# Optimization experiments

Hardware: AMD Instinct MI355X
Metric: run time of the kernel (lower is better)

## Reference

```python
import jax, jax.numpy as jnp
import numpy as np

STATE_DIM = 32
CONTROL_DIM = 8
EMBED_DIM = 96
LATENT_DIM = STATE_DIM + EMBED_DIM  # 128
HIDDEN = 512
B, M = 2048, 64


def setup_inputs() -> dict:
    key = jax.random.key(0)
    ks = jax.random.split(key, 16)
    s = lambda k, shp, fan: jax.random.normal(k, shp, jnp.float32) * (1.0 / np.sqrt(fan))
    return {
        "x_k": jax.random.normal(ks[0], (B, STATE_DIM), jnp.float32),
        "u_seq": jax.random.normal(ks[1], (B, M, CONTROL_DIM), jnp.float32),
        "x_next_seq": jax.random.normal(ks[2], (B, M, STATE_DIM), jnp.float32),
        # encoder MLP (depth=3): in->h, h->h, h->h, h->embed
        "W1": s(ks[3], (STATE_DIM, HIDDEN), STATE_DIM), "b1": jnp.zeros((HIDDEN,), jnp.float32),
        "W2": s(ks[4], (HIDDEN, HIDDEN), HIDDEN), "b2": jnp.zeros((HIDDEN,), jnp.float32),
        "W3": s(ks[5], (HIDDEN, HIDDEN), HIDDEN), "b3": jnp.zeros((HIDDEN,), jnp.float32),
        "Wo": s(ks[6], (HIDDEN, EMBED_DIM), HIDDEN), "bo": jnp.zeros((EMBED_DIM,), jnp.float32),
        # Koopman operators (Linear, no bias); stored as [in, out]
        "A": s(ks[7], (LATENT_DIM, LATENT_DIM), LATENT_DIM),
        "Bmat": s(ks[8], (CONTROL_DIM, LATENT_DIM), CONTROL_DIM),
    }


def _encode(x, W1, b1, W2, b2, W3, b3, Wo, bo):
    h = jax.nn.relu(x @ W1 + b1)
    h = jax.nn.relu(h @ W2 + b2)
    h = jax.nn.relu(h @ W3 + b3)
    return h @ Wo + bo


def _lift(x, W1, b1, W2, b2, W3, b3, Wo, bo):
    return jnp.concatenate([x, _encode(x, W1, b1, W2, b2, W3, b3, Wo, bo)], axis=-1)


def reference(x_k, u_seq, x_next_seq, W1, b1, W2, b2, W3, b3, Wo, bo, A, Bmat):
    m = u_seq.shape[1]
    z_k = _lift(x_k, W1, b1, W2, b2, W3, b3, Wo, bo)  # [B, L]
    # lift targets (encoder applied to flattened [B*M, S])
    z_target_seq = _lift(x_next_seq.reshape(-1, STATE_DIM), W1, b1, W2, b2, W3, b3, Wo, bo)
    z_target_seq = z_target_seq.reshape(-1, m, LATENT_DIM)
    # precompute control contributions, then sequential LTI recurrence via scan
    bu = jnp.einsum('bmc,cl->mbl', u_seq, Bmat)  # [M, B, L]

    def step(z, bu_i):
        z_next = z @ A + bu_i
        return z_next, z_next

    _, z_pred = jax.lax.scan(step, z_k, bu)  # [M, B, L]
    z_pred_seq = jnp.transpose(z_pred, (1, 0, 2))  # [B, M, L]
    x_pred_seq = z_pred_seq[..., :STATE_DIM]
    return (z_pred_seq, x_pred_seq, z_target_seq)
```

## Files before the change

kernel.cpp:

```cpp
#include <hip/hip_runtime.h>


typedef unsigned short u16;
typedef __attribute__((ext_vector_type(8))) short bf16x8;
typedef __attribute__((ext_vector_type(4))) short bf16x4;
typedef __attribute__((ext_vector_type(4))) float f32x4;

#define OFF_W1 0
#define OFF_W2 16384
#define OFF_W3 278528
#define OFF_WO 540672
#define OFF_ZK_BYTES 1179648
#define OFF_AH 1114112
#define OFF_AL 1130496

#define XPRED_OFF 16777216
#define ZTGT_OFF  20971520

__device__ __forceinline__ float bf2f(u16 u) {
  unsigned int i = ((unsigned int)u) << 16;
  return __builtin_bit_cast(float, i);
}
__device__ __forceinline__ u16 f2bf(float f) {
  unsigned int i = __builtin_bit_cast(unsigned int, f);
  i = (i + 0x7FFFu + ((i >> 16) & 1u)) >> 16;
  return (u16)i;
}

__global__ void prep_swizzle(const float* __restrict__ W1, const float* __restrict__ W2,
                             const float* __restrict__ W3, const float* __restrict__ Wo,
                             const float* __restrict__ Am, u16* __restrict__ dst) {
  int f = blockIdx.x;
  int l = threadIdx.x;
  const float* src; int K, N; u16* d; int lo = 0;
  if (f < 32)        { src = W1; K = 32;  N = 512; d = dst + OFF_W1; }
  else if (f < 544)  { src = W2; K = 512; N = 512; d = dst + OFF_W2; f -= 32; }
  else if (f < 1056) { src = W3; K = 512; N = 512; d = dst + OFF_W3; f -= 544; }
  else if (f < 1152) { src = Wo; K = 512; N = 96;  d = dst + OFF_WO; f -= 1056; }
  else if (f < 1184) { src = Am; K = 128; N = 128; d = dst + OFF_AH; f -= 1152; }
  else               { src = Am; K = 128; N = 128; d = dst + OFF_AL; f -= 1184; lo = 1; }
  const int KF = K >> 5;
  const int ct = f / KF, ks = f - ct * KF;
  const int q = l >> 4, n = l & 15;
  const int kbase = ks * 32 + q * 8;
  const int col = ct * 16 + n;
  bf16x8 vh;
  #pragma unroll
  for (int j = 0; j < 8; ++j) {
    float v = src[(size_t)(kbase + j) * N + col];
    u16 h = f2bf(v);
    if (lo) h = f2bf(v - bf2f(h));
    vh[j] = (short)h;
  }
  *(bf16x8*)(d + ((size_t)f * 64 + l) * 8) = vh;
}

__device__ __forceinline__ void store_h(const f32x4 (&acc)[4][4],
                                        const float* __restrict__ bias,
                                        u16* hbuf, int rh, int cg, int q, int n) {
  __syncthreads();
  #pragma unroll
  for (int i = 0; i < 4; ++i) {
    const int col = cg * 64 + i * 16 + n;
    const float bia = bias[col];
    #pragma unroll
    for (int rg = 0; rg < 4; ++rg) {
      const int rb = rh * 64 + rg * 16 + q * 4;
      float f0 = fmaxf(acc[rg][i][0] + bia, 0.f);
      float f1 = fmaxf(acc[rg][i][1] + bia, 0.f);
      float f2 = fmaxf(acc[rg][i][2] + bia, 0.f);
      float f3 = fmaxf(acc[rg][i][3] + bia, 0.f);
      unsigned p01, p23;
      asm("v_cvt_pk_bf16_f32 %0, %1, %2" : "=v"(p01) : "v"(f0), "v"(f1));
      asm("v_cvt_pk_bf16_f32 %0, %1, %2" : "=v"(p23) : "v"(f2), "v"(f3));
      hbuf[((rb + 0) * 512 + col) ^ (((rb + 0) & 7) << 3)] = (u16)(p01 & 0xFFFFu);
      hbuf[((rb + 1) * 512 + col) ^ (((rb + 1) & 7) << 3)] = (u16)(p01 >> 16);
      hbuf[((rb + 2) * 512 + col) ^ (((rb + 2) & 7) << 3)] = (u16)(p23 & 0xFFFFu);
      hbuf[((rb + 3) * 512 + col) ^ (((rb + 3) & 7) << 3)] = (u16)(p23 >> 16);
    }
  }
  __syncthreads();
}

__device__ __forceinline__ void big_layer(const u16* __restrict__ wb,
                                          const float* __restrict__ bias,
                                          u16* hbuf, int rh, int cg, int l, int q, int n) {
  f32x4 acc[4][4];
  #pragma unroll
  for (int rg = 0; rg < 4; ++rg)
    #pragma unroll
    for (int i = 0; i < 4; ++i) acc[rg][i] = (f32x4){0.f, 0.f, 0.f, 0.f};
  #pragma unroll 2
  for (int ks = 0; ks < 16; ++ks) {
    bf16x8 b[4], a[4];
    #pragma unroll
    for (int i = 0; i < 4; ++i)
      b[i] = *(const bf16x8*)(wb + (size_t)((4 * cg + i) * 16 + ks) * 512 + (size_t)l * 8);
    #pragma unroll
    for (int rg = 0; rg < 4; ++rg) {
      const int row = rh * 64 + rg * 16 + n;
      a[rg] = *(const bf16x8*)&hbuf[(row * 512 + ks * 32 + q * 8) ^ ((row & 7) << 3)];
    }
    #pragma unroll
    for (int rg = 0; rg < 4; ++rg)
      #pragma unroll
      for (int i = 0; i < 4; ++i)
        acc[rg][i] = __builtin_amdgcn_mfma_f32_16x16x32_bf16(a[rg], b[i], acc[rg][i], 0, 0, 0);
  }
  store_h(acc, bias, hbuf, rh, cg, q, n);
}

__global__ __launch_bounds__(1024) void encoder_tgt(
    const float* __restrict__ xnext, const u16* __restrict__ wf,
    const float* __restrict__ b1, const float* __restrict__ b2,
    const float* __restrict__ b3, const float* __restrict__ bo_,
    float* __restrict__ ztgt) {
  __shared__ __align__(16) u16 hbuf[128 * 512];
  const int tid = threadIdx.x;
  const int wv = tid >> 6, l = tid & 63;
  const int q = l >> 4, n = l & 15;
  const int rh = wv >> 3, cg = wv & 7;
  const size_t row0 = (size_t)blockIdx.x * 128;

  {
    const int r = tid >> 3, k0 = (tid & 7) * 4;
    f32x4 x = *(const f32x4*)(xnext + (row0 + r) * 32 + k0);
    *(f32x4*)(ztgt + (row0 + r) * 128 + k0) = x;
    bf16x4 v;
    #pragma unroll
    for (int j = 0; j < 4; ++j) v[j] = (short)f2bf(x[j]);
    *(bf16x4*)&hbuf[(r * 512 + k0) ^ ((r & 7) << 3)] = v;
  }
  __syncthreads();

  {
    f32x4 acc[4][4];
    #pragma unroll
    for (int rg = 0; rg < 4; ++rg)
      #pragma unroll
      for (int i = 0; i < 4; ++i) acc[rg][i] = (f32x4){0.f, 0.f, 0.f, 0.f};
    bf16x8 a[4];
    #pragma unroll
    for (int rg = 0; rg < 4; ++rg) {
      const int row = rh * 64 + rg * 16 + n;
      a[rg] = *(const bf16x8*)&hbuf[(row * 512 + q * 8) ^ ((row & 7) << 3)];
    }
    #pragma unroll
    for (int i = 0; i < 4; ++i) {
      bf16x8 b = *(const bf16x8*)(wf + OFF_W1 + (size_t)(4 * cg + i) * 512 + (size_t)l * 8);
      #pragma unroll
      for (int rg = 0; rg < 4; ++rg)
        acc[rg][i] = __builtin_amdgcn_mfma_f32_16x16x32_bf16(a[rg], b, acc[rg][i], 0, 0, 0);
    }
    store_h(acc, b1, hbuf, rh, cg, q, n);
  }

  big_layer(wf + OFF_W2, b2, hbuf, rh, cg, l, q, n);
  big_layer(wf + OFF_W3, b3, hbuf, rh, cg, l, q, n);

  if (cg < 6) {
    f32x4 o[4];
    #pragma unroll
    for (int rg = 0; rg < 4; ++rg) o[rg] = (f32x4){0.f, 0.f, 0.f, 0.f};
    #pragma unroll 2
    for (int ks = 0; ks < 16; ++ks) {
      bf16x8 b = *(const bf16x8*)(wf + OFF_WO + (size_t)(cg * 16 + ks) * 512 + (size_t)l * 8);
      #pragma unroll
      for (int rg = 0; rg < 4; ++rg) {
        const int row = rh * 64 + rg * 16 + n;
        bf16x8 a = *(const bf16x8*)&hbuf[(row * 512 + ks * 32 + q * 8) ^ ((row & 7) << 3)];
        o[rg] = __builtin_amdgcn_mfma_f32_16x16x32_bf16(a, b, o[rg], 0, 0, 0);
      }
    }
    const float bia = bo_[cg * 16 + n];
    #pragma unroll
    for (int rg = 0; rg < 4; ++rg)
      #pragma unroll
      for (int r = 0; r < 4; ++r)
        ztgt[(row0 + rh * 64 + rg * 16 + q * 4 + r) * 128 + 32 + cg * 16 + n] = o[rg][r] + bia;
  }
}

__global__ __launch_bounds__(512) void encoder_zk_f32(
    const float* __restrict__ xk,
    const float* __restrict__ W1, const float* __restrict__ b1,
    const float* __restrict__ W2, const float* __restrict__ b2,
    const float* __restrict__ W3, const float* __restrict__ b3,
    const float* __restrict__ Wo, const float* __restrict__ bo_,
    float* __restrict__ zk_out) {
  __shared__ __align__(16) float hb[2][8][512];
  __shared__ __align__(16) float xb[8][32];
  const int t = threadIdx.x;
  const int row0 = blockIdx.x * 8;
  if (t < 256) {
    int r = t >> 5, j = t & 31;
    float v = xk[(size_t)(row0 + r) * 32 + j];
    xb[r][j] = v;
    zk_out[(size_t)(row0 + r) * 128 + j] = v;
  }
  __syncthreads();
  const int c = t;
  {
    float a[8];
    const float i0 = b1[c];
    #pragma unroll
    for (int r = 0; r < 8; ++r) a[r] = i0;
    for (int k = 0; k < 32; k += 4) {
      float w0 = W1[(size_t)(k+0)*512 + c];
      float w1 = W1[(size_t)(k+1)*512 + c];
      float w2 = W1[(size_t)(k+2)*512 + c];
      float w3 = W1[(size_t)(k+3)*512 + c];
      #pragma unroll
      for (int r = 0; r < 8; ++r) {
        f32x4 z = *(const f32x4*)&xb[r][k];
        a[r] += z[0]*w0 + z[1]*w1 + z[2]*w2 + z[3]*w3;
      }
    }
    #pragma unroll
    for (int r = 0; r < 8; ++r) hb[0][r][c] = fmaxf(a[r], 0.f);
  }
  __syncthreads();
  #pragma unroll
  for (int lyr = 0; lyr < 2; ++lyr) {
    const float* W = lyr ? W3 : W2;
    const float* bb = lyr ? b3 : b2;
    const float (*hin)[512] = hb[lyr & 1];
    float (*hout)[512] = hb[(lyr & 1) ^ 1];
    float a[8];
    const float i0 = bb[c];
    #pragma unroll
    for (int r = 0; r < 8; ++r) a[r] = i0;
    for (int k = 0; k < 512; k += 4) {
      float w0 = W[(size_t)(k+0)*512 + c];
      float w1 = W[(size_t)(k+1)*512 + c];
      float w2 = W[(size_t)(k+2)*512 + c];
      float w3 = W[(size_t)(k+3)*512 + c];
      #pragma unroll
      for (int r = 0; r < 8; ++r) {
        f32x4 z = *(const f32x4*)&hin[r][k];
        a[r] += z[0]*w0 + z[1]*w1 + z[2]*w2 + z[3]*w3;
      }
    }
    #pragma unroll
    for (int r = 0; r < 8; ++r) hout[r][c] = fmaxf(a[r], 0.f);
    __syncthreads();
  }
  if (t < 96) {
    float a[8];
    const float i0 = bo_[t];
    #pragma unroll
    for (int r = 0; r < 8; ++r) a[r] = i0;
    for (int k = 0; k < 512; k += 4) {
      float w0 = Wo[(size_t)(k+0)*96 + t];
      float w1 = Wo[(size_t)(k+1)*96 + t];
      float w2 = Wo[(size_t)(k+2)*96 + t];
      float w3 = Wo[(size_t)(k+3)*96 + t];
      #pragma unroll
      for (int r = 0; r < 8; ++r) {
        f32x4 z = *(const f32x4*)&hb[0][r][k];
        a[r] += z[0]*w0 + z[1]*w1 + z[2]*w2 + z[3]*w3;
      }
    }
    #pragma unroll
    for (int r = 0; r < 8; ++r)
      zk_out[(size_t)(row0 + r) * 128 + 32 + t] = a[r];
  }
}

__global__ __launch_bounds__(256) void scan_mfma(
    const float* __restrict__ zk, const u16* __restrict__ wf,
    const float* __restrict__ Bm, const float* __restrict__ useq,
    float* __restrict__ zpred, float* __restrict__ xpred) {
  __shared__ __align__(16) u16 ahf[32 * 512];
  __shared__ __align__(16) u16 alf[32 * 512];
  __shared__ __align__(16) float ubuf[8 * 512];
  __shared__ __align__(16) float zbuf[8][132];
  __shared__ __align__(16) u16 zh[16][136];
  __shared__ __align__(16) u16 zl[16][136];
  __shared__ __align__(16) float bu[8][132];
  const int t = threadIdx.x;
  const int wv = t >> 6, l = t & 63;
  const int q = l >> 4, n = l & 15;
  const size_t b0 = (size_t)blockIdx.x * 8;

  #pragma unroll
  for (int i = 0; i < 8; ++i) {
    const int f = wv * 8 + i;
    __builtin_amdgcn_global_load_lds(
        (const __attribute__((address_space(1))) unsigned int*)(wf + OFF_AH + (size_t)f * 512 + l * 8),
        (__attribute__((address_space(3))) unsigned int*)(ahf + (size_t)f * 512), 16, 0, 0);
    __builtin_amdgcn_global_load_lds(
        (const __attribute__((address_space(1))) unsigned int*)(wf + OFF_AL + (size_t)f * 512 + l * 8),
        (__attribute__((address_space(3))) unsigned int*)(alf + (size_t)f * 512), 16, 0, 0);
  }
  {
    const float* us = useq + b0 * 512;
    #pragma unroll
    for (int i = 0; i < 4; ++i)
      *(f32x4*)&ubuf[i * 1024 + t * 4] = *(const f32x4*)(us + i * 1024 + t * 4);
  }
  const int crow = t >> 5, cc0 = (t & 31) * 4;
  *(f32x4*)&zbuf[crow][cc0] = *(const f32x4*)(zk + (b0 + crow) * 128 + cc0);
  for (int i = t; i < 8 * 136; i += 256) { (&zh[8][0])[i] = 0; (&zl[8][0])[i] = 0; }
  f32x4 bmr[8];
  #pragma unroll
  for (int j = 0; j < 8; ++j) bmr[j] = *(const f32x4*)(Bm + (size_t)j * 128 + cc0);
  __syncthreads();

  const int ct0 = 2 * wv, ct1 = 2 * wv + 1;
  for (int s = 0; s < 64; ++s) {
    {
      f32x4 z = *(const f32x4*)&zbuf[crow][cc0];
      bf16x4 vh, vl;
      #pragma unroll
      for (int i = 0; i < 4; ++i) {
        u16 h = f2bf(z[i]);
        vh[i] = (short)h;
        vl[i] = (short)f2bf(z[i] - bf2f(h));
      }
      *(bf16x4*)&zh[crow][cc0] = vh;
      *(bf16x4*)&zl[crow][cc0] = vl;
      f32x4 uu0 = *(const f32x4*)&ubuf[crow * 512 + s * 8];
      f32x4 uu1 = *(const f32x4*)&ubuf[crow * 512 + s * 8 + 4];
      f32x4 bv = uu0[0] * bmr[0];
      bv += uu0[1] * bmr[1]; bv += uu0[2] * bmr[2]; bv += uu0[3] * bmr[3];
      bv += uu1[0] * bmr[4]; bv += uu1[1] * bmr[5]; bv += uu1[2] * bmr[6]; bv += uu1[3] * bmr[7];
      *(f32x4*)&bu[crow][cc0] = bv;
    }
    __syncthreads();
    f32x4 acc0 = {0.f, 0.f, 0.f, 0.f};
    f32x4 acc1 = {0.f, 0.f, 0.f, 0.f};
    #pragma unroll
    for (int ks = 0; ks < 4; ++ks) {
      const int ko = ks * 32 + q * 8;
      bf16x8 azh = *(const bf16x8*)&zh[n][ko];
      bf16x8 azl = *(const bf16x8*)&zl[n][ko];
      bf16x8 bh0 = *(const bf16x8*)&ahf[(size_t)(ct0 * 4 + ks) * 512 + l * 8];
      bf16x8 bl0 = *(const bf16x8*)&alf[(size_t)(ct0 * 4 + ks) * 512 + l * 8];
      bf16x8 bh1 = *(const bf16x8*)&ahf[(size_t)(ct1 * 4 + ks) * 512 + l * 8];
      bf16x8 bl1 = *(const bf16x8*)&alf[(size_t)(ct1 * 4 + ks) * 512 + l * 8];
      acc0 = __builtin_amdgcn_mfma_f32_16x16x32_bf16(azh, bh0, acc0, 0, 0, 0);
      acc0 = __builtin_amdgcn_mfma_f32_16x16x32_bf16(azl, bh0, acc0, 0, 0, 0);
      acc0 = __builtin_amdgcn_mfma_f32_16x16x32_bf16(azh, bl0, acc0, 0, 0, 0);
      acc1 = __builtin_amdgcn_mfma_f32_16x16x32_bf16(azh, bh1, acc1, 0, 0, 0);
      acc1 = __builtin_amdgcn_mfma_f32_16x16x32_bf16(azl, bh1, acc1, 0, 0, 0);
      acc1 = __builtin_amdgcn_mfma_f32_16x16x32_bf16(azh, bl1, acc1, 0, 0, 0);
    }
    if (q < 2) {
      #pragma unroll
      for (int r = 0; r < 4; ++r) {
        const int row = q * 4 + r;
        const int c0 = ct0 * 16 + n, c1 = ct1 * 16 + n;
        const float v0 = acc0[r] + bu[row][c0];
        const float v1 = acc1[r] + bu[row][c1];
        zbuf[row][c0] = v0;
        zbuf[row][c1] = v1;
        const size_t go = (b0 + row) * 64 + s;
        zpred[go * 128 + c0] = v0;
        zpred[go * 128 + c1] = v1;
        if (wv == 0) {
          xpred[go * 32 + c0] = v0;
          xpred[go * 32 + c1] = v1;
        }
      }
    }
    __syncthreads();
  }
}

extern "C" void kernel_launch(void* const* d_in, const int* in_sizes, int n_in,
                              void* d_out, int out_size, void* d_ws, size_t ws_size,
                              hipStream_t stream) {
  (void)in_sizes; (void)n_in; (void)out_size; (void)ws_size;
  const float* xk    = (const float*)d_in[0];
  const float* useq  = (const float*)d_in[1];
  const float* xnext = (const float*)d_in[2];
  const float* W1 = (const float*)d_in[3];
  const float* b1 = (const float*)d_in[4];
  const float* W2 = (const float*)d_in[5];
  const float* b2 = (const float*)d_in[6];
  const float* W3 = (const float*)d_in[7];
  const float* b3 = (const float*)d_in[8];
  const float* Wo = (const float*)d_in[9];
  const float* bo = (const float*)d_in[10];
  const float* A  = (const float*)d_in[11];
  const float* Bm = (const float*)d_in[12];

  float* out   = (float*)d_out;
  float* zpred = out;
  float* xpred = out + XPRED_OFF;
  float* ztgt  = out + ZTGT_OFF;
  u16*   wf    = (u16*)d_ws;
  float* zkw   = (float*)((char*)d_ws + OFF_ZK_BYTES);

  prep_swizzle<<<1216, 64, 0, stream>>>(W1, W2, W3, Wo, A, wf);
  encoder_zk_f32<<<256, 512, 0, stream>>>(xk, W1, b1, W2, b2, W3, b3, Wo, bo, zkw);
  scan_mfma<<<256, 256, 0, stream>>>(zkw, wf, Bm, useq, zpred, xpred);
  encoder_tgt<<<1024, 1024, 0, stream>>>(xnext, wf, b1, b2, b3, bo, ztgt);
}
```

Baseline: 559.8 us.

## Enlarge encoder per-wave tiles to 4x8 and spread scan across 8 waves

The target encoder now runs 512 threads per block, and each wave computes a 64x128 output tile, so every loaded weight and activation fragment feeds more MFMAs and LDS and global reads per FLOP drop. The output projection is reorganised so six waves each cover all 128 rows. The scan kernel moves to 512 threads with one column tile per wave, and its three split-bf16 MFMA products go into independent accumulators to shorten the dependency chain. The risks are fewer resident waves to hide latency in the encoder, since LDS use still allows only one block per CU, and higher register pressure from the larger accumulator arrays.

Result: faster. 522.5 us (-6.7%).

```diff
diff --git a/kernel.cpp b/kernel.cpp
--- a/kernel.cpp
+++ b/kernel.cpp
@@ -55,13 +55,13 @@
   *(bf16x8*)(d + ((size_t)f * 64 + l) * 8) = vh;
 }
 
-__device__ __forceinline__ void store_h(const f32x4 (&acc)[4][4],
+__device__ __forceinline__ void store_h(const f32x4 (&acc)[4][8],
                                         const float* __restrict__ bias,
                                         u16* hbuf, int rh, int cg, int q, int n) {
   __syncthreads();
   #pragma unroll
-  for (int i = 0; i < 4; ++i) {
-    const int col = cg * 64 + i * 16 + n;
+  for (int i = 0; i < 8; ++i) {
+    const int col = cg * 128 + i * 16 + n;
     const float bia = bias[col];
     #pragma unroll
     for (int rg = 0; rg < 4; ++rg) {
@@ -85,17 +85,17 @@
 __device__ __forceinline__ void big_layer(const u16* __restrict__ wb,
                                           const float* __restrict__ bias,
                                           u16* hbuf, int rh, int cg, int l, int q, int n) {
-  f32x4 acc[4][4];
+  f32x4 acc[4][8];
   #pragma unroll
   for (int rg = 0; rg < 4; ++rg)
     #pragma unroll
-    for (int i = 0; i < 4; ++i) acc[rg][i] = (f32x4){0.f, 0.f, 0.f, 0.f};
+    for (int i = 0; i < 8; ++i) acc[rg][i] = (f32x4){0.f, 0.f, 0.f, 0.f};
   #pragma unroll 2
   for (int ks = 0; ks < 16; ++ks) {
-    bf16x8 b[4], a[4];
-    #pragma unroll
-    for (int i = 0; i < 4; ++i)
-      b[i] = *(const bf16x8*)(wb + (size_t)((4 * cg + i) * 16 + ks) * 512 + (size_t)l * 8);
+    bf16x8 b[8], a[4];
+    #pragma unroll
+    for (int i = 0; i < 8; ++i)
+      b[i] = *(const bf16x8*)(wb + (size_t)((8 * cg + i) * 16 + ks) * 512 + (size_t)l * 8);
     #pragma unroll
     for (int rg = 0; rg < 4; ++rg) {
       const int row = rh * 64 + rg * 16 + n;
@@ -104,13 +104,13 @@
     #pragma unroll
     for (int rg = 0; rg < 4; ++rg)
       #pragma unroll
-      for (int i = 0; i < 4; ++i)
+      for (int i = 0; i < 8; ++i)
         acc[rg][i] = __builtin_amdgcn_mfma_f32_16x16x32_bf16(a[rg], b[i], acc[rg][i], 0, 0, 0);
   }
   store_h(acc, bias, hbuf, rh, cg, q, n);
 }
 
-__global__ __launch_bounds__(1024) void encoder_tgt(
+__global__ __launch_bounds__(512, 2) void encoder_tgt(
     const float* __restrict__ xnext, const u16* __restrict__ wf,
     const float* __restrict__ b1, const float* __restrict__ b2,
     const float* __restrict__ b3, const float* __restrict__ bo_,
@@ -119,26 +119,28 @@
   const int tid = threadIdx.x;
   const int wv = tid >> 6, l = tid & 63;
   const int q = l >> 4, n = l & 15;
-  const int rh = wv >> 3, cg = wv & 7;
+  const int rh = wv >> 2, cg = wv & 3;
   const size_t row0 = (size_t)blockIdx.x * 128;
 
   {
-    const int r = tid >> 3, k0 = (tid & 7) * 4;
-    f32x4 x = *(const f32x4*)(xnext + (row0 + r) * 32 + k0);
-    *(f32x4*)(ztgt + (row0 + r) * 128 + k0) = x;
-    bf16x4 v;
-    #pragma unroll
-    for (int j = 0; j < 4; ++j) v[j] = (short)f2bf(x[j]);
-    *(bf16x4*)&hbuf[(r * 512 + k0) ^ ((r & 7) << 3)] = v;
+    const int r = tid >> 2, k0 = (tid & 3) * 8;
+    f32x4 x0 = *(const f32x4*)(xnext + (row0 + r) * 32 + k0);
+    f32x4 x1 = *(const f32x4*)(xnext + (row0 + r) * 32 + k0 + 4);
+    *(f32x4*)(ztgt + (row0 + r) * 128 + k0)     = x0;
+    *(f32x4*)(ztgt + (row0 + r) * 128 + k0 + 4) = x1;
+    bf16x8 v;
+    #pragma unroll
+    for (int j = 0; j < 4; ++j) { v[j] = (short)f2bf(x0[j]); v[4 + j] = (short)f2bf(x1[j]); }
+    *(bf16x8*)&hbuf[(r * 512 + k0) ^ ((r & 7) << 3)] = v;
   }
   __syncthreads();
 
   {
-    f32x4 acc[4][4];
+    f32x4 acc[4][8];
     #pragma unroll
     for (int rg = 0; rg < 4; ++rg)
       #pragma unroll
-      for (int i = 0; i < 4; ++i) acc[rg][i] = (f32x4){0.f, 0.f, 0.f, 0.f};
+      for (int i = 0; i < 8; ++i) acc[rg][i] = (f32x4){0.f, 0.f, 0.f, 0.f};
     bf16x8 a[4];
     #pragma unroll
     for (int rg = 0; rg < 4; ++rg) {
@@ -146,8 +148,8 @@
       a[rg] = *(const bf16x8*)&hbuf[(row * 512 + q * 8) ^ ((row & 7) << 3)];
     }
     #pragma unroll
-    for (int i = 0; i < 4; ++i) {
-      bf16x8 b = *(const bf16x8*)(wf + OFF_W1 + (size_t)(4 * cg + i) * 512 + (size_t)l * 8);
+    for (int i = 0; i < 8; ++i) {
+      bf16x8 b = *(const bf16x8*)(wf + OFF_W1 + (size_t)(8 * cg + i) * 512 + (size_t)l * 8);
       #pragma unroll
       for (int rg = 0; rg < 4; ++rg)
         acc[rg][i] = __builtin_amdgcn_mfma_f32_16x16x32_bf16(a[rg], b, acc[rg][i], 0, 0, 0);
@@ -158,26 +160,26 @@
   big_layer(wf + OFF_W2, b2, hbuf, rh, cg, l, q, n);
   big_layer(wf + OFF_W3, b3, hbuf, rh, cg, l, q, n);
 
-  if (cg < 6) {
-    f32x4 o[4];
-    #pragma unroll
-    for (int rg = 0; rg < 4; ++rg) o[rg] = (f32x4){0.f, 0.f, 0.f, 0.f};
+  if (wv < 6) {
+    f32x4 o[8];
+    #pragma unroll
+    for (int rg = 0; rg < 8; ++rg) o[rg] = (f32x4){0.f, 0.f, 0.f, 0.f};
     #pragma unroll 2
     for (int ks = 0; ks < 16; ++ks) {
-      bf16x8 b = *(const bf16x8*)(wf + OFF_WO + (size_t)(cg * 16 + ks) * 512 + (size_t)l * 8);
-      #pragma unroll
-      for (int rg = 0; rg < 4; ++rg) {
-        const int row = rh * 64 + rg * 16 + n;
+      bf16x8 b = *(const bf16x8*)(wf + OFF_WO + (size_t)(wv * 16 + ks) * 512 + (size_t)l * 8);
+      #pragma unroll
+      for (int rg = 0; rg < 8; ++rg) {
+        const int row = rg * 16 + n;
         bf16x8 a = *(const bf16x8*)&hbuf[(row * 512 + ks * 32 + q * 8) ^ ((row & 7) << 3)];
         o[rg] = __builtin_amdgcn_mfma_f32_16x16x32_bf16(a, b, o[rg], 0, 0, 0);
       }
     }
-    const float bia = bo_[cg * 16 + n];
-    #pragma unroll
-    for (int rg = 0; rg < 4; ++rg)
+    const float bia = bo_[wv * 16 + n];
+    #pragma unroll
+    for (int rg = 0; rg < 8; ++rg)
       #pragma unroll
       for (int r = 0; r < 4; ++r)
-        ztgt[(row0 + rh * 64 + rg * 16 + q * 4 + r) * 128 + 32 + cg * 16 + n] = o[rg][r] + bia;
+        ztgt[(row0 + rg * 16 + q * 4 + r) * 128 + 32 + wv * 16 + n] = o[rg][r] + bia;
   }
 }
 
@@ -267,7 +269,7 @@
   }
 }
 
-__global__ __launch_bounds__(256) void scan_mfma(
+__global__ __launch_bounds__(512) void scan_mfma(
     const float* __restrict__ zk, const u16* __restrict__ wf,
     const float* __restrict__ Bm, const float* __restrict__ useq,
     float* __restrict__ zpred, float* __restrict__ xpred) {
@@ -284,8 +286,8 @@
   const size_t b0 = (size_t)blockIdx.x * 8;
 
   #pragma unroll
-  for (int i = 0; i < 8; ++i) {
-    const int f = wv * 8 + i;
+  for (int i = 0; i < 4; ++i) {
+    const int f = wv * 4 + i;
     __builtin_amdgcn_global_load_lds(
         (const __attribute__((address_space(1))) unsigned int*)(wf + OFF_AH + (size_t)f * 512 + l * 8),
         (__attribute__((address_space(3))) unsigned int*)(ahf + (size_t)f * 512), 16, 0, 0);
@@ -295,73 +297,65 @@
   }
   {
     const float* us = useq + b0 * 512;
-    #pragma unroll
-    for (int i = 0; i < 4; ++i)
-      *(f32x4*)&ubuf[i * 1024 + t * 4] = *(const f32x4*)(us + i * 1024 + t * 4);
-  }
-  const int crow = t >> 5, cc0 = (t & 31) * 4;
-  *(f32x4*)&zbuf[crow][cc0] = *(const f32x4*)(zk + (b0 + crow) * 128 + cc0);
-  for (int i = t; i < 8 * 136; i += 256) { (&zh[8][0])[i] = 0; (&zl[8][0])[i] = 0; }
-  f32x4 bmr[8];
-  #pragma unroll
-  for (int j = 0; j < 8; ++j) bmr[j] = *(const f32x4*)(Bm + (size_t)j * 128 + cc0);
-  __syncthreads();
-
-  const int ct0 = 2 * wv, ct1 = 2 * wv + 1;
+    *(f32x4*)&ubuf[t * 8]     = *(const f32x4*)(us + t * 8);
+    *(f32x4*)&ubuf[t * 8 + 4] = *(const f32x4*)(us + t * 8 + 4);
+  }
+  if (t < 256) {
+    const int r = t >> 5, c4 = (t & 31) * 4;
+    *(f32x4*)&zbuf[r][c4] = *(const f32x4*)(zk + (b0 + r) * 128 + c4);
+  }
+  for (int i = t; i < 8 * 136; i += 512) { (&zh[8][0])[i] = 0; (&zl[8][0])[i] = 0; }
+  float bm0[8], bm1[8];
+  #pragma unroll
+  for (int j = 0; j < 8; ++j) {
+    bm0[j] = Bm[(size_t)j * 128 + 2 * l];
+    bm1[j] = Bm[(size_t)j * 128 + 2 * l + 1];
+  }
+  __syncthreads();
+
   for (int s = 0; s < 64; ++s) {
     {
-      f32x4 z = *(const f32x4*)&zbuf[crow][cc0];
-      bf16x4 vh, vl;
-      #pragma unroll
-      for (int i = 0; i < 4; ++i) {
-        u16 h = f2bf(z[i]);
-        vh[i] = (short)h;
-        vl[i] = (short)f2bf(z[i] - bf2f(h));
-      }
-      *(bf16x4*)&zh[crow][cc0] = vh;
-      *(bf16x4*)&zl[crow][cc0] = vl;
-      f32x4 uu0 = *(const f32x4*)&ubuf[crow * 512 + s * 8];
-      f32x4 uu1 = *(const f32x4*)&ubuf[crow * 512 + s * 8 + 4];
-      f32x4 bv = uu0[0] * bmr[0];
-      bv += uu0[1] * bmr[1]; bv += uu0[2] * bmr[2]; bv += uu0[3] * bmr[3];
-      bv += uu1[0] * bmr[4]; bv += uu1[1] * bmr[5]; bv += uu1[2] * bmr[6]; bv += uu1[3] * bmr[7];
-      *(f32x4*)&bu[crow][cc0] = bv;
+      float z0 = zbuf[wv][2 * l], z1 = zbuf[wv][2 * l + 1];
+      u16 h0 = f2bf(z0), h1 = f2bf(z1);
+      u16 lo0 = f2bf(z0 - bf2f(h0)), lo1 = f2bf(z1 - bf2f(h1));
+      *(unsigned int*)&zh[wv][2 * l] = (unsigned int)h0 | ((unsigned int)h1 << 16);
+      *(unsigned int*)&zl[wv][2 * l] = (unsigned int)lo0 | ((unsigned int)lo1 << 16);
+      f32x4 ua = *(const f32x4*)&ubuf[wv * 512 + s * 8];
+      f32x4 ub = *(const f32x4*)&ubuf[wv * 512 + s * 8 + 4];
+      float bv0 = ua[0]*bm0[0] + ua[1]*bm0[1] + ua[2]*bm0[2] + ua[3]*bm0[3]
+                + ub[0]*bm0[4] + ub[1]*bm0[5] + ub[2]*bm0[6] + ub[3]*bm0[7];
+      float bv1 = ua[0]*bm1[0] + ua[1]*bm1[1] + ua[2]*bm1[2] + ua[3]*bm1[3]
+                + ub[0]*bm1[4] + ub[1]*bm1[5] + ub[2]*bm1[6] + ub[3]*bm1[7];
+      bu[wv][2 * l]     = bv0;
+      bu[wv][2 * l + 1] = bv1;
     }
     __syncthreads();
-    f32x4 acc0 = {0.f, 0.f, 0.f, 0.f};
-    f32x4 acc1 = {0.f, 0.f, 0.f, 0.f};
+    f32x4 aH = {0.f, 0.f, 0.f, 0.f};
+    f32x4 aL = {0.f, 0.f, 0.f, 0.f};
+    f32x4 aM = {0.f, 0.f, 0.f, 0.f};
     #pragma unroll
     for (int ks = 0; ks < 4; ++ks) {
       const int ko = ks * 32 + q * 8;
       bf16x8 azh = *(const bf16x8*)&zh[n][ko];
       bf16x8 azl = *(const bf16x8*)&zl[n][ko];
-      bf16x8 bh0 = *(const bf16x8*)&ahf[(size_t)(ct0 * 4 + ks) * 512 + l * 8];
-      bf16x8 bl0 = *(const bf16x8*)&alf[(size_t)(ct0 * 4 + ks) * 512 + l * 8];
-      bf16x8 bh1 = *(const bf16x8*)&ahf[(size_t)(ct1 * 4 + ks) * 512 + l * 8];
-      bf16x8 bl1 = *(const bf16x8*)&alf[(size_t)(ct1 * 4 + ks) * 512 + l * 8];
-      acc0 = __builtin_amdgcn_mfma_f32_16x16x32_bf16(azh, bh0, acc0, 0, 0, 0);
-      acc0 = __builtin_amdgcn_mfma_f32_16x16x32_bf16(azl, bh0, acc0, 0, 0, 0);
-      acc0 = __builtin_amdgcn_mfma_f32_16x16x32_bf16(azh, bl0, acc0, 0, 0, 0);
-      acc1 = __builtin_amdgcn_mfma_f32_16x16x32_bf16(azh, bh1, acc1, 0, 0, 0);
-      acc1 = __builtin_amdgcn_mfma_f32_16x16x32_bf16(azl, bh1, acc1, 0, 0, 0);
-      acc1 = __builtin_amdgcn_mfma_f32_16x16x32_bf16(azh, bl1, acc1, 0, 0, 0);
-    }
+      bf16x8 bh = *(const bf16x8*)&ahf[(size_t)(wv * 4 + ks) * 512 + l * 8];
+      bf16x8 bl = *(const bf16x8*)&alf[(size_t)(wv * 4 + ks) * 512 + l * 8];
+      aH = __builtin_amdgcn_mfma_f32_16x16x32_bf16(azh, bh, aH, 0, 0, 0);
+      aL = __builtin_amdgcn_mfma_f32_16x16x32_bf16(azl, bh, aL, 0, 0, 0);
+      aM = __builtin_amdgcn_mfma_f32_16x16x32_bf16(azh, bl, aM, 0, 0, 0);
+    }
+    f32x4 acc = aH + aL;
+    acc = acc + aM;
     if (q < 2) {
       #pragma unroll
       for (int r = 0; r < 4; ++r) {
         const int row = q * 4 + r;
-        const int c0 = ct0 * 16 + n, c1 = ct1 * 16 + n;
-        const float v0 = acc0[r] + bu[row][c0];
-        const float v1 = acc1[r] + bu[row][c1];
-        zbuf[row][c0] = v0;
-        zbuf[row][c1] = v1;
+        const int c = wv * 16 + n;
+        const float v = acc[r] + bu[row][c];
+        zbuf[row][c] = v;
         const size_t go = (b0 + row) * 64 + s;
-        zpred[go * 128 + c0] = v0;
-        zpred[go * 128 + c1] = v1;
-        if (wv == 0) {
-          xpred[go * 32 + c0] = v0;
-          xpred[go * 32 + c1] = v1;
-        }
+        zpred[go * 128 + c] = v;
+        if (wv < 2) xpred[go * 32 + c] = v;
       }
     }
     __syncthreads();
@@ -395,6 +389,6 @@
 
   prep_swizzle<<<1216, 64, 0, stream>>>(W1, W2, W3, Wo, A, wf);
   encoder_zk_f32<<<256, 512, 0, stream>>>(xk, W1, b1, W2, b2, W3, b3, Wo, bo, zkw);
-  scan_mfma<<<256, 256, 0, stream>>>(zkw, wf, Bm, useq, zpred, xpred);
-  encoder_tgt<<<1024, 1024, 0, stream>>>(xnext, wf, b1, b2, b3, bo, ztgt);
-}
+  scan_mfma<<<256, 512, 0, stream>>>(zkw, wf, Bm, useq, zpred, xpred);
+  encoder_tgt<<<1024, 512, 0, stream>>>(xnext, wf, b1, b2, b3, bo, ztgt);
+}
```
